# Kernel tuning notes

Hardware: AMD Instinct MI355X
Metric: run time of the kernel (lower is better)

The kernel has to match this reference:

```python
import jax, jax.numpy as jnp
import numpy as np

N_SAMPLES = 128
AGENTS = 64
D = 128          # latent_size
EDIM = 2         # edge attr dim
N = N_SAMPLES * AGENTS
EPS = 1e-5


def _build_edges():
    a = np.arange(AGENTS)
    rows = np.repeat(a, AGENTS)
    cols = np.tile(a, AGENTS)
    mask = rows != cols  # fully connected, no self loops
    rows, cols = rows[mask], cols[mask]
    offsets = (np.arange(N_SAMPLES) * AGENTS)[:, None]
    src = (rows[None, :] + offsets).ravel().astype(np.int32)  # edge_index[0]
    dst = (cols[None, :] + offsets).ravel().astype(np.int32)  # edge_index[1]
    return src, dst


def setup_inputs() -> dict:
    key = jax.random.key(0)
    ks = jax.random.split(key, 16)
    src, dst = _build_edges()
    zin = 2 * D + EDIM  # CGConv concat [x_i, x_j, e]
    inp = {
        "gnn_in": jax.random.normal(ks[0], (N, D), jnp.float32),
        "centers": jax.random.normal(ks[1], (N, EDIM), jnp.float32),
        "edge_src": jnp.asarray(src),
        "edge_dst": jnp.asarray(dst),
    }
    for li, base in ((1, 2), (2, 8)):
        inp[f"Wf{li}"] = jax.random.normal(ks[base + 0], (zin, D), jnp.float32) / np.sqrt(zin)
        inp[f"bf{li}"] = jnp.zeros((D,), jnp.float32)
        inp[f"Ws{li}"] = jax.random.normal(ks[base + 1], (zin, D), jnp.float32) / np.sqrt(zin)
        inp[f"bs{li}"] = jnp.zeros((D,), jnp.float32)
        inp[f"gamma{li}"] = jnp.ones((D,), jnp.float32)
        inp[f"beta{li}"] = jnp.zeros((D,), jnp.float32)
    return inp


def _cgconv(x, e, src, dst, Wf, bf, Ws, bs, gamma, beta):
    # message: z = [x_i(target), x_j(source), e]; sigmoid(Wf z) * softplus(Ws z)
    z = jnp.concatenate([x[dst], x[src], e], axis=-1)  # [E, 2D+2]
    m = jax.nn.sigmoid(z @ Wf + bf) * jax.nn.softplus(z @ Ws + bs)
    agg = jax.ops.segment_sum(m, dst, num_segments=N)  # scatter-add at targets
    # batch norm (training-mode batch stats) then residual, as in PyG CGConv
    mu = agg.mean(axis=0)
    var = agg.var(axis=0)
    agg = (agg - mu) * jax.lax.rsqrt(var + EPS) * gamma + beta
    return agg + x


def reference(gnn_in, centers, edge_src, edge_dst,
              Wf1, bf1, Ws1, bs1, gamma1, beta1,
              Wf2, bf2, Ws2, bs2, gamma2, beta2):
    # edge_attr = centers[col] - centers[row]
    e = centers[edge_dst] - centers[edge_src]  # [E, 2]
    x = jax.nn.relu(_cgconv(gnn_in, e, edge_src, edge_dst, Wf1, bf1, Ws1, bs1, gamma1, beta1))
    x = jax.nn.relu(_cgconv(x, e, edge_src, edge_dst, Wf2, bf2, Ws2, bs2, gamma2, beta2))
    return x
```

## Files before the change

kernel.cpp:

```cpp
#include <hip/hip_runtime.h>
#include <hip/hip_bf16.h>

#define NSAMP 128
#define AGENTS 64
#define D 128
#define NN (NSAMP * AGENTS)
#define LOG2E 1.44269504088896340736f
#define LN2   0.69314718055994530942f
#define EPSF  1e-5f

typedef __attribute__((ext_vector_type(8))) short short8;
typedef __attribute__((ext_vector_type(4))) float floatx4;

__device__ __forceinline__ float u2f(unsigned v) {
    float f; __builtin_memcpy(&f, &v, 4); return f;
}
__device__ __forceinline__ unsigned f2u(float f) {
    unsigned v; __builtin_memcpy(&v, &f, 4); return v;
}
__device__ __forceinline__ unsigned short f2bf(float f) {
    unsigned x; __builtin_memcpy(&x, &f, 4);
    return (unsigned short)((x + 0x7FFFu + ((x >> 16) & 1u)) >> 16);
}

__device__ __forceinline__ void stats_tree(
    unsigned int (*EApk)[17], unsigned int (*EBpk)[17],
    int cl, int slot, int c, float s1, float s2, float* __restrict__ sc)
{
    __syncthreads();
    EApk[slot][cl] = f2u(s1);
    EBpk[slot][cl] = f2u(s2);
    __syncthreads();
    #pragma unroll
    for (int off = 8; off >= 1; off >>= 1) {
        if (slot < off) {
            EApk[slot][cl] = f2u(u2f(EApk[slot][cl]) + u2f(EApk[slot + off][cl]));
            EBpk[slot][cl] = f2u(u2f(EBpk[slot][cl]) + u2f(EBpk[slot + off][cl]));
        }
        __syncthreads();
    }
    if (slot == 0) {
        atomicAdd(&sc[c],       u2f(EApk[0][cl]));
        atomicAdd(&sc[128 + c], u2f(EBpk[0][cl]));
    }
}

template<int LAYER>
__global__ __launch_bounds__(256, 4) void prep_half(
    const float* __restrict__ xin,
    const float* __restrict__ agg_in,
    const float* __restrict__ centers,
    const float* __restrict__ Wf, const float* __restrict__ bf_,
    const float* __restrict__ Ws, const float* __restrict__ bs_,
    const float* __restrict__ gm_prev, const float* __restrict__ bt_prev,
    const float* __restrict__ sacc_prev,
    float* __restrict__ agg_out, float* __restrict__ sacc_out)
{
    const int bid = blockIdx.x;
    const int xcd = bid & 7;
    const int tmp = bid >> 3;
    const int inner = tmp & 15;
    const int s = ((tmp >> 4) << 3) + xcd;
    const int q = inner >> 1, h = inner & 1;

    const int nbase = s * AGENTS;
    const int tid = threadIdx.x, w = tid >> 6, lane = tid & 63;
    const int quad = lane >> 4, l16 = lane & 15;
    const int col = q * 16 + l16;

    __shared__ __align__(16) unsigned short WL[4][16][136];
    __shared__ unsigned int EApk[32][17];
    __shared__ unsigned int EBpk[64][17];
    __shared__ float bnA[128], bnB[128];

    {
        const int arr = tid >> 6, klane = tid & 63;
        const int wcol = klane & 15, kg = klane >> 4;
        const float* M = (arr < 2) ? Wf : Ws;
        const int side = arr & 1;
        const float* src = M + (size_t)(side * 128 + kg * 32) * D + q * 16 + wcol;
        #pragma unroll
        for (int u = 0; u < 16; ++u) {
            float f0 = src[(size_t)(2 * u) * D];
            float f1 = src[(size_t)(2 * u + 1) * D];
            unsigned pk = (unsigned)f2bf(f0) | ((unsigned)f2bf(f1) << 16);
            *(unsigned*)&WL[arr][wcol][kg * 32 + 2 * u] = pk;
        }
    }
    if (LAYER == 2) {
        if (tid < 128) {
            const float inv = 1.f / NN;
            float mu = sacc_prev[tid] * inv;
            float var = sacc_prev[128 + tid] * inv - mu * mu;
            float rs = rsqrtf(var + EPSF);
            float A = rs * gm_prev[tid];
            bnA[tid] = A;
            bnB[tid] = fmaf(-mu, A, bt_prev[tid]);
        }
    }
    __syncthreads();

    short8 a[4];
    if (LAYER == 1) {
        const float* xr = xin + (size_t)(nbase + w * 16 + l16) * D + quad * 8;
        #pragma unroll
        for (int kc = 0; kc < 4; ++kc) {
            float4 v0 = *(const float4*)(xr + kc * 32);
            float4 v1 = *(const float4*)(xr + kc * 32 + 4);
            short8 t;
            t[0] = (short)f2bf(v0.x); t[1] = (short)f2bf(v0.y);
            t[2] = (short)f2bf(v0.z); t[3] = (short)f2bf(v0.w);
            t[4] = (short)f2bf(v1.x); t[5] = (short)f2bf(v1.y);
            t[6] = (short)f2bf(v1.z); t[7] = (short)f2bf(v1.w);
            a[kc] = t;
        }
    } else {
        const size_t ro = (size_t)(nbase + w * 16 + l16) * D + quad * 8;
        #pragma unroll
        for (int kc = 0; kc < 4; ++kc) {
            int cc = quad * 8 + kc * 32;
            float4 g0 = *(const float4*)&agg_in[ro + kc * 32];
            float4 g1 = *(const float4*)&agg_in[ro + kc * 32 + 4];
            float4 x0v = *(const float4*)(xin + ro + kc * 32);
            float4 x1v = *(const float4*)(xin + ro + kc * 32 + 4);
            float4 A0 = *(const float4*)&bnA[cc], A1 = *(const float4*)&bnA[cc + 4];
            float4 B0 = *(const float4*)&bnB[cc], B1 = *(const float4*)&bnB[cc + 4];
            short8 t;
            t[0] = (short)f2bf(fmaxf(0.f, fmaf(g0.x, A0.x, B0.x) + x0v.x));
            t[1] = (short)f2bf(fmaxf(0.f, fmaf(g0.y, A0.y, B0.y) + x0v.y));
            t[2] = (short)f2bf(fmaxf(0.f, fmaf(g0.z, A0.z, B0.z) + x0v.z));
            t[3] = (short)f2bf(fmaxf(0.f, fmaf(g0.w, A0.w, B0.w) + x0v.w));
            t[4] = (short)f2bf(fmaxf(0.f, fmaf(g1.x, A1.x, B1.x) + x1v.x));
            t[5] = (short)f2bf(fmaxf(0.f, fmaf(g1.y, A1.y, B1.y) + x1v.y));
            t[6] = (short)f2bf(fmaxf(0.f, fmaf(g1.z, A1.z, B1.z) + x1v.z));
            t[7] = (short)f2bf(fmaxf(0.f, fmaf(g1.w, A1.w, B1.w) + x1v.w));
            a[kc] = t;
        }
    }

    const int doEA = ((w >> 1) == h);
    floatx4 accB[2];
    #pragma unroll
    for (int a2 = 0; a2 < 2; ++a2) {
        const int arr = 1 + 2 * a2;
        floatx4 ac = {0.f, 0.f, 0.f, 0.f};
        #pragma unroll
        for (int kc = 0; kc < 4; ++kc)
            ac = __builtin_amdgcn_mfma_f32_16x16x32_bf16(
                a[kc], *(const short8*)&WL[arr][l16][quad * 8 + kc * 32], ac, 0, 0, 0);
        accB[a2] = ac;
    }
    floatx4 accA[2] = {{0,0,0,0},{0,0,0,0}};
    if (doEA) {
        #pragma unroll
        for (int a2 = 0; a2 < 2; ++a2) {
            const int arr = 2 * a2;
            floatx4 ac = {0.f, 0.f, 0.f, 0.f};
            #pragma unroll
            for (int kc = 0; kc < 4; ++kc)
                ac = __builtin_amdgcn_mfma_f32_16x16x32_bf16(
                    a[kc], *(const short8*)&WL[arr][l16][quad * 8 + kc * 32], ac, 0, 0, 0);
            accA[a2] = ac;
        }
    }
    const float cwf0 = Wf[256 * D + col], cwf1 = Wf[257 * D + col];
    const float cws0 = Ws[256 * D + col], cws1 = Ws[257 * D + col];
    const float bfv = bf_[col], bsv = bs_[col];
    #pragma unroll
    for (int r = 0; r < 4; ++r) {
        int row = w * 16 + quad * 4 + r;
        int n = nbase + row;
        float ce0 = centers[2 * n], ce1 = centers[2 * n + 1];
        float ctf = fmaf(ce0, cwf0, ce1 * cwf1);
        float cts = fmaf(ce0, cws0, ce1 * cws1);
        unsigned ebf = (unsigned)f2bf(__builtin_amdgcn_exp2f(-LOG2E * (accB[0][r] - ctf)));
        unsigned ebs = (unsigned)f2bf(__builtin_amdgcn_exp2f( LOG2E * (accB[1][r] - cts)));
        EBpk[row][l16] = ebf | (ebs << 16);
        if (doEA) {
            unsigned eaf = (unsigned)f2bf(__builtin_amdgcn_exp2f(-LOG2E * (accA[0][r] + ctf + bfv)));
            unsigned eas = (unsigned)f2bf(__builtin_amdgcn_exp2f( LOG2E * (accA[1][r] + cts + bsv)));
            EApk[(w & 1) * 16 + quad * 4 + r][l16] = eaf | (eas << 16);
        }
    }
    __syncthreads();

    const int cl = tid & 15, slot = tid >> 4;
    const int c = q * 16 + cl;
    float eaf[2], eas[2], ac2[2];
    #pragma unroll
    for (int i = 0; i < 2; ++i) {
        unsigned pk = EApk[slot * 2 + i][cl];
        eaf[i] = u2f(pk << 16);
        eas[i] = u2f(pk & 0xFFFF0000u);
        ac2[i] = 0.f;
    }
    #pragma unroll
    for (int jb = 0; jb < 64; jb += 8) {
        float af[16], as_[16];
        #pragma unroll
        for (int u = 0; u < 8; ++u) {
            unsigned pk = EBpk[jb + u][cl];
            float ebf = u2f(pk << 16);
            float ebs = u2f(pk & 0xFFFF0000u);
            af[u * 2 + 0] = fmaf(eaf[0], ebf, 1.f);
            af[u * 2 + 1] = fmaf(eaf[1], ebf, 1.f);
            as_[u * 2 + 0] = fmaf(eas[0], ebs, 1.f);
            as_[u * 2 + 1] = fmaf(eas[1], ebs, 1.f);
        }
        float sg[16], lg[16];
        #pragma unroll
        for (int u = 0; u < 16; ++u) {
            asm volatile("v_rcp_f32 %0, %1" : "=v"(sg[u]) : "v"(af[u]));
            asm volatile("v_log_f32 %0, %1" : "=v"(lg[u]) : "v"(as_[u]));
        }
        #pragma unroll
        for (int u = 0; u < 16; ++u)
            ac2[u & 1] = fmaf(sg[u], lg[u], ac2[u & 1]);
    }
    float s1 = 0.f, s2 = 0.f;
    #pragma unroll
    for (int i = 0; i < 2; ++i) {
        int d = h * 32 + slot * 2 + i;
        unsigned pk = EBpk[d][cl];
        float ebf = u2f(pk << 16);
        float ebs = u2f(pk & 0xFFFF0000u);
        float sg = __builtin_amdgcn_rcpf(fmaf(eaf[i], ebf, 1.f));
        float lg = __builtin_amdgcn_logf(fmaf(eas[i], ebs, 1.f));
        float v = (ac2[i] - sg * lg) * LN2;
        agg_out[(size_t)(nbase + d) * D + c] = v;
        s1 += v; s2 += v * v;
    }
    stats_tree(EApk, EBpk, cl, slot, c, s1, s2, sacc_out);
}

__global__ __launch_bounds__(256) void final_bn(
    const float* __restrict__ x0, const float* __restrict__ agg1,
    const float* __restrict__ agg2, const float* __restrict__ sacc,
    const float* __restrict__ gm1, const float* __restrict__ bt1,
    const float* __restrict__ gm2, const float* __restrict__ bt2,
    float* __restrict__ outp)
{
    const int tid = threadIdx.x;
    __shared__ float bnA[128], bnB[128], bn2A[128], bn2B[128];
    if (tid < 128) {
        const float inv = 1.f / NN;
        float mu = sacc[tid] * inv;
        float var = sacc[128 + tid] * inv - mu * mu;
        float rs = rsqrtf(var + EPSF);
        float A = rs * gm1[tid];
        bnA[tid] = A;
        bnB[tid] = fmaf(-mu, A, bt1[tid]);
        float mu2 = sacc[256 + tid] * inv;
        float var2 = sacc[384 + tid] * inv - mu2 * mu2;
        float rs2 = rsqrtf(var2 + EPSF);
        float A2 = rs2 * gm2[tid];
        bn2A[tid] = A2;
        bn2B[tid] = fmaf(-mu2, A2, bt2[tid]);
    }
    __syncthreads();
    const int bid = blockIdx.x;
    const int s = ((bid >> 5) << 3) + (bid & 7);
    const int inner = (bid >> 3) & 3;
    const int t = (s * 4 + inner) * 256 + tid;
    const int n = t >> 4, c8 = (t & 15) * 8;
    size_t off = (size_t)n * D + c8;
    float o[8];
    #pragma unroll
    for (int hh = 0; hh < 2; ++hh) {
        float4 g2 = *(const float4*)&agg2[off + hh * 4];
        float4 g1 = *(const float4*)&agg1[off + hh * 4];
        float4 xv = *(const float4*)&x0[off + hh * 4];
        int cc = c8 + hh * 4;
        o[hh*4+0] = fmaxf(0.f, fmaf(g2.x, bn2A[cc+0], bn2B[cc+0]) +
                    fmaxf(0.f, fmaf(g1.x, bnA[cc+0], bnB[cc+0]) + xv.x));
        o[hh*4+1] = fmaxf(0.f, fmaf(g2.y, bn2A[cc+1], bn2B[cc+1]) +
                    fmaxf(0.f, fmaf(g1.y, bnA[cc+1], bnB[cc+1]) + xv.y));
        o[hh*4+2] = fmaxf(0.f, fmaf(g2.z, bn2A[cc+2], bn2B[cc+2]) +
                    fmaxf(0.f, fmaf(g1.z, bnA[cc+2], bnB[cc+2]) + xv.z));
        o[hh*4+3] = fmaxf(0.f, fmaf(g2.w, bn2A[cc+3], bn2B[cc+3]) +
                    fmaxf(0.f, fmaf(g1.w, bnA[cc+3], bnB[cc+3]) + xv.w));
    }
    *(float4*)&outp[off]     = *(float4*)&o[0];
    *(float4*)&outp[off + 4] = *(float4*)&o[4];
}

extern "C" void kernel_launch(void* const* d_in, const int* in_sizes, int n_in,
                              void* d_out, int out_size, void* d_ws, size_t ws_size,
                              hipStream_t stream) {
    const float* x0      = (const float*)d_in[0];
    const float* centers = (const float*)d_in[1];
    const float* Wf1 = (const float*)d_in[4];
    const float* bf1 = (const float*)d_in[5];
    const float* Ws1 = (const float*)d_in[6];
    const float* bs1 = (const float*)d_in[7];
    const float* gm1 = (const float*)d_in[8];
    const float* bt1 = (const float*)d_in[9];
    const float* Wf2 = (const float*)d_in[10];
    const float* bf2 = (const float*)d_in[11];
    const float* Ws2 = (const float*)d_in[12];
    const float* bs2 = (const float*)d_in[13];
    const float* gm2 = (const float*)d_in[14];
    const float* bt2 = (const float*)d_in[15];

    const size_t ND = (size_t)NN * D;
    float* agg1 = (float*)d_ws;
    float* agg2 = agg1 + ND;
    float* sacc = agg1 + 2 * ND;
    float* outp = (float*)d_out;

    hipMemsetAsync(sacc, 0, 512 * sizeof(float), stream);

    prep_half<1><<<dim3(2048), dim3(256), 0, stream>>>(
        x0, agg1 , centers, Wf1, bf1, Ws1, bs1,
        gm1 , bt1 , sacc , agg1, sacc);

    prep_half<2><<<dim3(2048), dim3(256), 0, stream>>>(
        x0, agg1, centers, Wf2, bf2, Ws2, bs2,
        gm1, bt1, sacc, agg2, sacc + 256);

    final_bn<<<dim3(512), dim3(256), 0, stream>>>(
        x0, agg1, agg2, sacc, gm1, bt1, gm2, bt2, outp);
}
```

Baseline: 150.5 us.

## Replace BN-stat atomics with per-block partials and software reciprocal

Each block now writes its per-channel sum and sum-of-squares partials to a dedicated slot instead of doing atomicAdd into a shared accumulator, which also removes the memset. Consumer kernels reduce the 256 partial rows per channel themselves, and layer-2 block 0 publishes the layer-1 BN coefficients for the final kernel. The hardware v_rcp in the inner loop is replaced with a bit-trick initial guess plus two Newton iterations. The trade is less atomic contention and one fewer launch against every block of the next kernel redundantly reading 256KB of partials, plus extra VALU work for the reciprocal.

```diff
diff --git a/kernel.cpp b/kernel.cpp
--- a/kernel.cpp
+++ b/kernel.cpp
@@ -8,6 +8,7 @@
 #define LOG2E 1.44269504088896340736f
 #define LN2   0.69314718055994530942f
 #define EPSF  1e-5f
+#define PACC_STRIDE 32768
 
 typedef __attribute__((ext_vector_type(8))) short short8;
 typedef __attribute__((ext_vector_type(4))) float floatx4;
@@ -22,10 +23,17 @@
     unsigned x; __builtin_memcpy(&x, &f, 4);
     return (unsigned short)((x + 0x7FFFu + ((x >> 16) & 1u)) >> 16);
 }
+__device__ __forceinline__ float rcp_fast(float t) {
+    float r = u2f(0x7EF311C3u - f2u(t));
+    r = r * fmaf(-t, r, 2.f);
+    r = r * fmaf(-t, r, 2.f);
+    return r;
+}
 
 __device__ __forceinline__ void stats_tree(
     unsigned int (*EApk)[17], unsigned int (*EBpk)[17],
-    int cl, int slot, int c, float s1, float s2, float* __restrict__ sc)
+    int cl, int slot, int c, int prow, float s1, float s2,
+    float* __restrict__ pacc)
 {
     __syncthreads();
     EApk[slot][cl] = f2u(s1);
@@ -40,8 +48,8 @@
         __syncthreads();
     }
     if (slot == 0) {
-        atomicAdd(&sc[c],       u2f(EApk[0][cl]));
-        atomicAdd(&sc[128 + c], u2f(EBpk[0][cl]));
+        pacc[prow * 128 + c]               = u2f(EApk[0][cl]);
+        pacc[PACC_STRIDE + prow * 128 + c] = u2f(EBpk[0][cl]);
     }
 }
 
@@ -53,8 +61,10 @@
     const float* __restrict__ Wf, const float* __restrict__ bf_,
     const float* __restrict__ Ws, const float* __restrict__ bs_,
     const float* __restrict__ gm_prev, const float* __restrict__ bt_prev,
-    const float* __restrict__ sacc_prev,
-    float* __restrict__ agg_out, float* __restrict__ sacc_out)
+    const float* __restrict__ pacc_prev,
+    float* __restrict__ agg_out,
+    float* __restrict__ pacc_out,
+    float* __restrict__ bn1_out)
 {
     const int bid = blockIdx.x;
     const int xcd = bid & 7;
@@ -72,6 +82,7 @@
     __shared__ unsigned int EApk[32][17];
     __shared__ unsigned int EBpk[64][17];
     __shared__ float bnA[128], bnB[128];
+    __shared__ float redS[2][2][128];
 
     {
         const int arr = tid >> 6, klane = tid & 63;
@@ -88,17 +99,40 @@
         }
     }
     if (LAYER == 2) {
+        const int c = tid & 127, hr = tid >> 7;
+        const float* pA = pacc_prev + (size_t)(hr * 128) * 128 + c;
+        const float* pB = pA + PACC_STRIDE;
+        float a0 = 0.f, a1 = 0.f, b0 = 0.f, b1 = 0.f;
+        #pragma unroll 4
+        for (int r = 0; r < 128; r += 2) {
+            a0 += pA[(size_t)r * 128];
+            a1 += pA[(size_t)(r + 1) * 128];
+            b0 += pB[(size_t)r * 128];
+            b1 += pB[(size_t)(r + 1) * 128];
+        }
+        redS[0][hr][c] = a0 + a1;
+        redS[1][hr][c] = b0 + b1;
+    }
+    __syncthreads();
+    if (LAYER == 2) {
         if (tid < 128) {
             const float inv = 1.f / NN;
-            float mu = sacc_prev[tid] * inv;
-            float var = sacc_prev[128 + tid] * inv - mu * mu;
+            float s1 = redS[0][0][tid] + redS[0][1][tid];
+            float s2 = redS[1][0][tid] + redS[1][1][tid];
+            float mu = s1 * inv;
+            float var = s2 * inv - mu * mu;
             float rs = rsqrtf(var + EPSF);
             float A = rs * gm_prev[tid];
+            float B = fmaf(-mu, A, bt_prev[tid]);
             bnA[tid] = A;
-            bnB[tid] = fmaf(-mu, A, bt_prev[tid]);
-        }
-    }
-    __syncthreads();
+            bnB[tid] = B;
+            if (bid == 0) {
+                bn1_out[tid]       = A;
+                bn1_out[128 + tid] = B;
+            }
+        }
+        __syncthreads();
+    }
 
     short8 a[4];
     if (LAYER == 1) {
@@ -210,7 +244,7 @@
         float sg[16], lg[16];
         #pragma unroll
         for (int u = 0; u < 16; ++u) {
-            asm volatile("v_rcp_f32 %0, %1" : "=v"(sg[u]) : "v"(af[u]));
+            sg[u] = rcp_fast(af[u]);
             asm volatile("v_log_f32 %0, %1" : "=v"(lg[u]) : "v"(as_[u]));
         }
         #pragma unroll
@@ -224,38 +258,56 @@
         unsigned pk = EBpk[d][cl];
         float ebf = u2f(pk << 16);
         float ebs = u2f(pk & 0xFFFF0000u);
-        float sg = __builtin_amdgcn_rcpf(fmaf(eaf[i], ebf, 1.f));
-        float lg = __builtin_amdgcn_logf(fmaf(eas[i], ebs, 1.f));
+        float af = fmaf(eaf[i], ebf, 1.f);
+        float as2 = fmaf(eas[i], ebs, 1.f);
+        float sg = rcp_fast(af);
+        float lg;
+        asm volatile("v_log_f32 %0, %1" : "=v"(lg) : "v"(as2));
         float v = (ac2[i] - sg * lg) * LN2;
         agg_out[(size_t)(nbase + d) * D + c] = v;
         s1 += v; s2 += v * v;
     }
-    stats_tree(EApk, EBpk, cl, slot, c, s1, s2, sacc_out);
+    stats_tree(EApk, EBpk, cl, slot, c, s * 2 + h, s1, s2, pacc_out);
 }
 
 __global__ __launch_bounds__(256) void final_bn(
     const float* __restrict__ x0, const float* __restrict__ agg1,
-    const float* __restrict__ agg2, const float* __restrict__ sacc,
-    const float* __restrict__ gm1, const float* __restrict__ bt1,
+    const float* __restrict__ agg2, const float* __restrict__ pacc2,
+    const float* __restrict__ bn1g,
     const float* __restrict__ gm2, const float* __restrict__ bt2,
     float* __restrict__ outp)
 {
     const int tid = threadIdx.x;
     __shared__ float bnA[128], bnB[128], bn2A[128], bn2B[128];
+    __shared__ float redS[2][2][128];
+    {
+        const int c = tid & 127, hr = tid >> 7;
+        const float* pA = pacc2 + (size_t)(hr * 128) * 128 + c;
+        const float* pB = pA + PACC_STRIDE;
+        float a0 = 0.f, a1 = 0.f, b0 = 0.f, b1 = 0.f;
+        #pragma unroll 4
+        for (int r = 0; r < 128; r += 2) {
+            a0 += pA[(size_t)r * 128];
+            a1 += pA[(size_t)(r + 1) * 128];
+            b0 += pB[(size_t)r * 128];
+            b1 += pB[(size_t)(r + 1) * 128];
+        }
+        redS[0][hr][c] = a0 + a1;
+        redS[1][hr][c] = b0 + b1;
+    }
+    __syncthreads();
     if (tid < 128) {
         const float inv = 1.f / NN;
-        float mu = sacc[tid] * inv;
-        float var = sacc[128 + tid] * inv - mu * mu;
+        float s1 = redS[0][0][tid] + redS[0][1][tid];
+        float s2 = redS[1][0][tid] + redS[1][1][tid];
+        float mu = s1 * inv;
+        float var = s2 * inv - mu * mu;
         float rs = rsqrtf(var + EPSF);
-        float A = rs * gm1[tid];
-        bnA[tid] = A;
-        bnB[tid] = fmaf(-mu, A, bt1[tid]);
-        float mu2 = sacc[256 + tid] * inv;
-        float var2 = sacc[384 + tid] * inv - mu2 * mu2;
-        float rs2 = rsqrtf(var2 + EPSF);
-        float A2 = rs2 * gm2[tid];
+        float A2 = rs * gm2[tid];
         bn2A[tid] = A2;
-        bn2B[tid] = fmaf(-mu2, A2, bt2[tid]);
+        bn2B[tid] = fmaf(-mu, A2, bt2[tid]);
+        bnA[tid] = bn1g[tid];
+        bnB[tid] = bn1g[128 + tid];
     }
     __syncthreads();
     const int bid = blockIdx.x;
@@ -303,21 +355,22 @@
     const float* bt2 = (const float*)d_in[15];
 
     const size_t ND = (size_t)NN * D;
-    float* agg1 = (float*)d_ws;
-    float* agg2 = agg1 + ND;
-    float* sacc = agg1 + 2 * ND;
-    float* outp = (float*)d_out;
-
-    hipMemsetAsync(sacc, 0, 512 * sizeof(float), stream);
+    float* agg1  = (float*)d_ws;
+    float* agg2  = agg1 + ND;
+    float* pacc1 = agg1 + 2 * ND;
+    float* pacc2 = pacc1 + 2 * PACC_STRIDE;
+    float* bn1g  = pacc2 + 2 * PACC_STRIDE;
+    float* outp  = (float*)d_out;
 
     prep_half<1><<<dim3(2048), dim3(256), 0, stream>>>(
         x0, agg1 , centers, Wf1, bf1, Ws1, bs1,
-        gm1 , bt1 , sacc , agg1, sacc);
+        gm1 , bt1 , pacc1 ,
+        agg1, pacc1, bn1g );
 
     prep_half<2><<<dim3(2048), dim3(256), 0, stream>>>(
         x0, agg1, centers, Wf2, bf2, Ws2, bs2,
-        gm1, bt1, sacc, agg2, sacc + 256);
+        gm1, bt1, pacc1, agg2, pacc2, bn1g);
 
     final_bn<<<dim3(512), dim3(256), 0, stream>>>(
-        x0, agg1, agg2, sacc, gm1, bt1, gm2, bt2, outp);
-}
+        x0, agg1, agg2, pacc2, bn1g, gm2, bt2, outp);
+}
```

Result: slower. 167.4 us (+11.2%).
